# Kernel tuning notes

Hardware: AMD Instinct MI355X
Metric: run time of the kernel (lower is better)

Reference implementation:

```python
import jax, jax.numpy as jnp
import numpy as np

B, LQ, LK, NF = 8, 8192, 1024, 64


def setup_inputs() -> dict:
    key = jax.random.key(0)
    k1, k2, k3, k4, k5 = jax.random.split(key, 5)
    x = jax.random.normal(k1, (B, LQ, NF), dtype=jnp.float32)
    kv = jax.random.normal(k2, (B, LK, NF), dtype=jnp.float32)
    # 1x1 submanifold convolutions == per-point linear maps (no bias)
    scale = 1.0 / np.sqrt(NF)
    Wq = jax.random.normal(k3, (NF, NF), dtype=jnp.float32) * scale
    Wk = jax.random.normal(k4, (NF, NF), dtype=jnp.float32) * scale
    Wv = jax.random.normal(k5, (NF, NF), dtype=jnp.float32) * scale
    return {"x": x, "kv": kv, "Wq": Wq, "Wk": Wk, "Wv": Wv}


def reference(x, kv, Wq, Wk, Wv):
    # q/k/v projections (1x1 convs on sparse features = dense matmuls)
    q = jnp.einsum("bqd,de->bqe", x, Wq)    # [B, LQ, NF]
    k = jnp.einsum("bkd,de->bke", kv, Wk)   # [B, LK, NF]
    v = jnp.einsum("bkd,de->bke", kv, Wv)   # [B, LK, NF]
    # per-batch (block-diagonal / ragged) attention: e = q k^T, softmax over keys, @ v
    scores = jnp.einsum("bqe,bke->bqk", q, k)        # [B, LQ, LK] (no scaling, as in source)
    attn = jax.nn.softmax(scores, axis=-1)
    out = jnp.einsum("bqk,bke->bqe", attn, v)        # [B, LQ, NF]
    return out
```

## Files before the change

kernel.cpp:

```cpp
#include <hip/hip_runtime.h>
#include <hip/hip_fp16.h>

constexpr int B_  = 8;
constexpr int LQ  = 8192;
constexpr int LK  = 1024;
constexpr int NF  = 64;
constexpr int PAD = 8;
constexpr int LDW = NF + PAD;

typedef _Float16 f16x8 __attribute__((ext_vector_type(8)));
typedef float    f32x4 __attribute__((ext_vector_type(4)));

#define MFMA16(a, b, c) __builtin_amdgcn_mfma_f32_16x16x32_f16((a), (b), (c), 0, 0, 0)

__device__ __forceinline__ f16x8 cvt8(const float* p) {
  float4 a = ((const float4*)p)[0];
  float4 b = ((const float4*)p)[1];
  f16x8 r;
  r[0] = (_Float16)a.x; r[1] = (_Float16)a.y; r[2] = (_Float16)a.z; r[3] = (_Float16)a.w;
  r[4] = (_Float16)b.x; r[5] = (_Float16)b.y; r[6] = (_Float16)b.z; r[7] = (_Float16)b.w;
  return r;
}

__device__ __forceinline__ f16x8 ldf(const _Float16* p) { return *(const f16x8*)p; }

__device__ __forceinline__ void st_pk4(_Float16* dst, float a, float b, float c, float d) {
  auto lo = __builtin_amdgcn_cvt_pkrtz(a, b);
  auto hi = __builtin_amdgcn_cvt_pkrtz(c, d);
  auto v  = __builtin_shufflevector(lo, hi, 0, 1, 2, 3);
  *(decltype(v)*)dst = v;
}

__device__ __forceinline__ f16x8 pack8(f32x4 u, f32x4 v) {
  auto a  = __builtin_amdgcn_cvt_pkrtz(u[0], u[1]);
  auto b  = __builtin_amdgcn_cvt_pkrtz(u[2], u[3]);
  auto cc = __builtin_amdgcn_cvt_pkrtz(v[0], v[1]);
  auto d  = __builtin_amdgcn_cvt_pkrtz(v[2], v[3]);
  f16x8 r;
  r[0] = a[0];  r[1] = a[1];  r[2] = b[0]; r[3] = b[1];
  r[4] = cc[0]; r[5] = cc[1]; r[6] = d[0]; r[7] = d[1];
  return r;
}

__device__ __forceinline__ void dma16(const _Float16* g, _Float16* l) {
  __builtin_amdgcn_global_load_lds(
      (const __attribute__((address_space(1))) unsigned int*)g,
      (__attribute__((address_space(3))) unsigned int*)l, 16, 0, 0);
}

__global__ __launch_bounds__(256) void kv_proj_kernel(
    const float* __restrict__ kv, const float* __restrict__ Wk,
    const float* __restrict__ Wv, _Float16* __restrict__ Kb,
    _Float16* __restrict__ Vt) {
  __shared__ __align__(16) _Float16 wkT[NF][LDW];
  __shared__ __align__(16) _Float16 wvT[NF][LDW];
  __shared__ __align__(16) _Float16 ktile[64][LDW];
  __shared__ __align__(16) _Float16 vtileT[64][LDW];

  const int t    = threadIdx.x;
  const int wave = t >> 6, lane = t & 63, g = lane >> 4, c = lane & 15;
  const int b    = blockIdx.x >> 4;
  const int key_base = (blockIdx.x & 15) * 64;

#pragma unroll
  for (int i = 0; i < 16; ++i) {
    int idx = t + 256 * i;
    int e = idx >> 6, d = idx & 63;
    wkT[d][e] = (_Float16)Wk[idx];
    wvT[d][e] = (_Float16)Wv[idx];
  }

  const float* src = kv + ((size_t)b * LK + key_base + wave * 16 + c) * NF;
  f16x8 a0 = cvt8(src + g * 8);
  f16x8 a1 = cvt8(src + 32 + g * 8);
  __syncthreads();

#pragma unroll
  for (int mb = 0; mb < 4; ++mb) {
    f32x4 kacc = {0.f, 0.f, 0.f, 0.f};
    const _Float16* wk0 = &wkT[mb * 16 + c][g * 8];
    kacc = MFMA16(ldf(wk0),      a0, kacc);
    kacc = MFMA16(ldf(wk0 + 32), a1, kacc);
    st_pk4(&ktile[wave * 16 + c][(8 * (mb >> 1) + 2 * g + (mb & 1)) * 4],
           kacc[0], kacc[1], kacc[2], kacc[3]);

    f32x4 vacc = {0.f, 0.f, 0.f, 0.f};
    const _Float16* wv0 = &wvT[mb * 16 + c][g * 8];
    vacc = MFMA16(a0, ldf(wv0),      vacc);
    vacc = MFMA16(a1, ldf(wv0 + 32), vacc);
    st_pk4(&vtileT[mb * 16 + c][(8 * (wave >> 1) + 2 * g + (wave & 1)) * 4],
           vacc[0], vacc[1], vacc[2], vacc[3]);
  }
  __syncthreads();

  _Float16* KbT = Kb + (size_t)blockIdx.x * 4096;
  _Float16* VbT = Vt + (size_t)blockIdx.x * 4096;
#pragma unroll
  for (int rep = 0; rep < 2; ++rep) {
    int q  = t + rep * 256;
    int li = q & 63;
    int gg = li >> 4, cc = li & 15;
    int kb = (q >> 6) & 3, h = q >> 8;
    *(f16x8*)(KbT + q * 8) = ldf(&ktile[kb * 16 + cc][32 * h + 8 * gg]);
    *(f16x8*)(VbT + q * 8) = ldf(&vtileT[kb * 16 + cc][32 * h + 8 * gg]);
  }
}

__global__ __launch_bounds__(256) void attn_kernel(
    const float* __restrict__ x, const float* __restrict__ Wq,
    const _Float16* __restrict__ Kb, const _Float16* __restrict__ Vt,
    float* __restrict__ out) {
  __shared__ __align__(16) _Float16 wq[NF][LDW];
  __shared__ __align__(16) _Float16 tiles[2][8192];

  const int t    = threadIdx.x;
  const int wave = t >> 6, lane = t & 63, g = lane >> 4, c = lane & 15;
  const int b    = blockIdx.x >> 6;
  const int q_base = (blockIdx.x & 63) * 128;
  constexpr float LOG2E = 1.44269504088896f;

  const _Float16* Kt = Kb + (size_t)b * 16 * 4096;
  const _Float16* Vg = Vt + (size_t)b * 16 * 4096;

#pragma unroll
  for (int i = 0; i < 16; ++i) {
    int idx = t + 256 * i;
    wq[idx & 63][idx >> 6] = (_Float16)(Wq[idx] * LOG2E);
  }

#pragma unroll
  for (int q = 0; q < 4; ++q) {
    int ch = wave * 4 + q;
    const _Float16* src = (ch < 8 ? Kt + ch * 512 : Vg + ch * 512 - 4096) + lane * 8;
    dma16(src, &tiles[0][ch * 512]);
  }
  __syncthreads();

  f16x8 qb[2][2];
#pragma unroll
  for (int s = 0; s < 2; ++s) {
    const float* xrow = x + ((size_t)b * LQ + q_base + wave * 32 + s * 16 + c) * NF;
    f16x8 xa0 = cvt8(xrow + g * 8);
    f16x8 xa1 = cvt8(xrow + 32 + g * 8);
    f32x4 qa[4];
#pragma unroll
    for (int mb = 0; mb < 4; ++mb) {
      qa[mb] = {0.f, 0.f, 0.f, 0.f};
      const _Float16* wq0 = &wq[mb * 16 + c][g * 8];
      qa[mb] = MFMA16(ldf(wq0),      xa0, qa[mb]);
      qa[mb] = MFMA16(ldf(wq0 + 32), xa1, qa[mb]);
    }
    qb[s][0] = pack8(qa[0], qa[1]);
    qb[s][1] = pack8(qa[2], qa[3]);
  }

  float m_s[2] = {-1e30f, -1e30f}, l_s[2] = {0.f, 0.f};
  f32x4 oacc[2][4];
#pragma unroll
  for (int s = 0; s < 2; ++s)
#pragma unroll
    for (int nb = 0; nb < 4; ++nb) oacc[s][nb] = {0.f, 0.f, 0.f, 0.f};

#pragma unroll 2
  for (int tile = 0; tile < 16; ++tile) {
    const int buf = tile & 1;
    if (tile < 15) {
      const _Float16* kn = Kt + (tile + 1) * 4096;
      const _Float16* vn = Vg + (tile + 1) * 4096;
#pragma unroll
      for (int q = 0; q < 4; ++q) {
        int ch = wave * 4 + q;
        const _Float16* src = (ch < 8 ? kn + ch * 512 : vn + ch * 512 - 4096) + lane * 8;
        dma16(src, &tiles[buf ^ 1][ch * 512]);
      }
    }
    const _Float16* tb = tiles[buf];

    f32x4 st[2][4];
#pragma unroll
    for (int kb = 0; kb < 4; ++kb) {
      f16x8 k0 = ldf(tb + (size_t)(kb * 64 + lane) * 8);
      f16x8 k1 = ldf(tb + (size_t)((kb + 4) * 64 + lane) * 8);
      st[0][kb] = {0.f, 0.f, 0.f, 0.f};
      st[1][kb] = {0.f, 0.f, 0.f, 0.f};
      st[0][kb] = MFMA16(k0, qb[0][0], st[0][kb]);
      st[0][kb] = MFMA16(k1, qb[0][1], st[0][kb]);
      st[1][kb] = MFMA16(k0, qb[1][0], st[1][kb]);
      st[1][kb] = MFMA16(k1, qb[1][1], st[1][kb]);
    }

    f16x8 pa[2][2];
#pragma unroll
    for (int s = 0; s < 2; ++s) {
      float tmax = st[s][0][0];
#pragma unroll
      for (int kb = 0; kb < 4; ++kb)
#pragma unroll
        for (int r = 0; r < 4; ++r) tmax = fmaxf(tmax, st[s][kb][r]);
      tmax = fmaxf(tmax, __shfl_xor(tmax, 16));
      tmax = fmaxf(tmax, __shfl_xor(tmax, 32));

      if (__ballot(tmax > m_s[s]) != 0) {
        float mnew  = fmaxf(m_s[s], tmax);
        float alpha = __builtin_amdgcn_exp2f(m_s[s] - mnew);
        m_s[s] = mnew;
        l_s[s] *= alpha;
        float aq[4];
#pragma unroll
        for (int r = 0; r < 4; ++r) aq[r] = __shfl(alpha, 4 * g + r);
#pragma unroll
        for (int nb = 0; nb < 4; ++nb)
#pragma unroll
          for (int r = 0; r < 4; ++r) oacc[s][nb][r] *= aq[r];
      }

      float rsum = 0.f;
#pragma unroll
      for (int kb = 0; kb < 4; ++kb)
#pragma unroll
        for (int r = 0; r < 4; ++r) {
          float p = __builtin_amdgcn_exp2f(st[s][kb][r] - m_s[s]);
          st[s][kb][r] = p;
          rsum += p;
        }
      rsum += __shfl_xor(rsum, 16);
      rsum += __shfl_xor(rsum, 32);
      l_s[s] += rsum;

      pa[s][0] = pack8(st[s][0], st[s][1]);
      pa[s][1] = pack8(st[s][2], st[s][3]);
    }

#pragma unroll
    for (int nb = 0; nb < 4; ++nb) {
      f16x8 v0 = ldf(tb + 4096 + (size_t)(nb * 64 + lane) * 8);
      f16x8 v1 = ldf(tb + 4096 + (size_t)((nb + 4) * 64 + lane) * 8);
      oacc[0][nb] = MFMA16(pa[0][0], v0, oacc[0][nb]);
      oacc[0][nb] = MFMA16(pa[0][1], v1, oacc[0][nb]);
      oacc[1][nb] = MFMA16(pa[1][0], v0, oacc[1][nb]);
      oacc[1][nb] = MFMA16(pa[1][1], v1, oacc[1][nb]);
    }
    __syncthreads();
  }

#pragma unroll
  for (int s = 0; s < 2; ++s) {
    float linv = 1.0f / l_s[s];
    float lq[4];
#pragma unroll
    for (int r = 0; r < 4; ++r) lq[r] = __shfl(linv, 4 * g + r);
#pragma unroll
    for (int nb = 0; nb < 4; ++nb)
#pragma unroll
      for (int r = 0; r < 4; ++r)
        out[((size_t)b * LQ + q_base + wave * 32 + s * 16 + 4 * g + r) * NF + nb * 16 + c] =
            oacc[s][nb][r] * lq[r];
  }
}

extern "C" void kernel_launch(void* const* d_in, const int* in_sizes, int n_in,
                              void* d_out, int out_size, void* d_ws, size_t ws_size,
                              hipStream_t stream) {
  const float* x  = (const float*)d_in[0];
  const float* kv = (const float*)d_in[1];
  const float* Wq = (const float*)d_in[2];
  const float* Wk = (const float*)d_in[3];
  const float* Wv = (const float*)d_in[4];
  float* out = (float*)d_out;

  _Float16* Kb = (_Float16*)d_ws;
  _Float16* Vt = Kb + (size_t)B_ * LK * NF;

  kv_proj_kernel<<<B_ * (LK / 64), 256, 0, stream>>>(kv, Wk, Wv, Kb, Vt);
  attn_kernel<<<B_ * (LQ / 128), 256, 0, stream>>>(x, Wq, Kb, Vt, out);
}
```

Measured before the change: 108.7 us.

## Use 128-key tiles with interleaved KV layout and MFMA row-sum

The projection kernel now writes K and V into one interleaved buffer laid out as 128-key tiles, so the attention kernel streams one contiguous 32KB chunk per tile and runs 8 iterations instead of 16. The softmax row sum is computed with an MFMA against a ones vector instead of scalar adds and cross-lane shuffles. The trailing __syncthreads is replaced by a waitcnt+barrier at loop start, and Wq staging reuses the second LDS buffer. The aim is fewer barriers and fewer rescale passes per key, plus less VALU and shuffle work, at the cost of more registers for larger score tiles and 64KB of LDS, which may lower occupancy.

```diff
diff --git a/kernel.cpp b/kernel.cpp
--- a/kernel.cpp
+++ b/kernel.cpp
@@ -48,10 +48,13 @@
       (__attribute__((address_space(3))) unsigned int*)l, 16, 0, 0);
 }
 
+__device__ __forceinline__ void tile_barrier() {
+  asm volatile("s_waitcnt vmcnt(0)\n\ts_barrier" ::: "memory");
+}
+
 __global__ __launch_bounds__(256) void kv_proj_kernel(
     const float* __restrict__ kv, const float* __restrict__ Wk,
-    const float* __restrict__ Wv, _Float16* __restrict__ Kb,
-    _Float16* __restrict__ Vt) {
+    const float* __restrict__ Wv, _Float16* __restrict__ KV) {
   __shared__ __align__(16) _Float16 wkT[NF][LDW];
   __shared__ __align__(16) _Float16 wvT[NF][LDW];
   __shared__ __align__(16) _Float16 ktile[64][LDW];
@@ -60,7 +63,8 @@
   const int t    = threadIdx.x;
   const int wave = t >> 6, lane = t & 63, g = lane >> 4, c = lane & 15;
   const int b    = blockIdx.x >> 4;
-  const int key_base = (blockIdx.x & 15) * 64;
+  const int t64  = blockIdx.x & 15;
+  const int key_base = t64 * 64;
 
 #pragma unroll
   for (int i = 0; i < 16; ++i) {
@@ -93,25 +97,25 @@
   }
   __syncthreads();
 
-  _Float16* KbT = Kb + (size_t)blockIdx.x * 4096;
-  _Float16* VbT = Vt + (size_t)blockIdx.x * 4096;
+  const int half = t64 & 1;
+  _Float16* base = KV + ((size_t)b * 8 + (t64 >> 1)) * 16384;
 #pragma unroll
   for (int rep = 0; rep < 2; ++rep) {
-    int q  = t + rep * 256;
-    int li = q & 63;
-    int gg = li >> 4, cc = li & 15;
-    int kb = (q >> 6) & 3, h = q >> 8;
-    *(f16x8*)(KbT + q * 8) = ldf(&ktile[kb * 16 + cc][32 * h + 8 * gg]);
-    *(f16x8*)(VbT + q * 8) = ldf(&vtileT[kb * 16 + cc][32 * h + 8 * gg]);
+    int q   = t + rep * 256;
+    int li  = q & 63;
+    int gg  = li >> 4, cc = li & 15;
+    int sub = (q >> 6) & 3, h = q >> 8;
+    int ck  = h * 8 + half * 4 + sub;
+    int cv  = (half * 2 + h) * 4 + sub;
+    *(f16x8*)(base + (ck * 64 + li) * 8)        = ldf(&ktile[sub * 16 + cc][32 * h + 8 * gg]);
+    *(f16x8*)(base + 8192 + (cv * 64 + li) * 8) = ldf(&vtileT[sub * 16 + cc][32 * h + 8 * gg]);
   }
 }
 
 __global__ __launch_bounds__(256) void attn_kernel(
     const float* __restrict__ x, const float* __restrict__ Wq,
-    const _Float16* __restrict__ Kb, const _Float16* __restrict__ Vt,
-    float* __restrict__ out) {
-  __shared__ __align__(16) _Float16 wq[NF][LDW];
-  __shared__ __align__(16) _Float16 tiles[2][8192];
+    const _Float16* __restrict__ KV, float* __restrict__ out) {
+  __shared__ __align__(16) _Float16 lds[2][16384];
 
   const int t    = threadIdx.x;
   const int wave = t >> 6, lane = t & 63, g = lane >> 4, c = lane & 15;
@@ -119,20 +123,18 @@
   const int q_base = (blockIdx.x & 63) * 128;
   constexpr float LOG2E = 1.44269504088896f;
 
-  const _Float16* Kt = Kb + (size_t)b * 16 * 4096;
-  const _Float16* Vg = Vt + (size_t)b * 16 * 4096;
-
+  _Float16* wqp = &lds[1][0];
 #pragma unroll
   for (int i = 0; i < 16; ++i) {
     int idx = t + 256 * i;
-    wq[idx & 63][idx >> 6] = (_Float16)(Wq[idx] * LOG2E);
-  }
-
-#pragma unroll
-  for (int q = 0; q < 4; ++q) {
-    int ch = wave * 4 + q;
-    const _Float16* src = (ch < 8 ? Kt + ch * 512 : Vg + ch * 512 - 4096) + lane * 8;
-    dma16(src, &tiles[0][ch * 512]);
+    wqp[(idx & 63) * LDW + (idx >> 6)] = (_Float16)(Wq[idx] * LOG2E);
+  }
+
+  const _Float16* Kt = KV + (size_t)b * 8 * 16384;
+#pragma unroll
+  for (int q = 0; q < 8; ++q) {
+    int ch = wave * 8 + q;
+    dma16(Kt + ch * 512 + lane * 8, &lds[0][ch * 512]);
   }
   __syncthreads();
 
@@ -146,7 +148,7 @@
 #pragma unroll
     for (int mb = 0; mb < 4; ++mb) {
       qa[mb] = {0.f, 0.f, 0.f, 0.f};
-      const _Float16* wq0 = &wq[mb * 16 + c][g * 8];
+      const _Float16* wq0 = &wqp[(mb * 16 + c) * LDW + g * 8];
       qa[mb] = MFMA16(ldf(wq0),      xa0, qa[mb]);
       qa[mb] = MFMA16(ldf(wq0 + 32), xa1, qa[mb]);
     }
@@ -154,33 +156,36 @@
     qb[s][1] = pack8(qa[2], qa[3]);
   }
 
-  float m_s[2] = {-1e30f, -1e30f}, l_s[2] = {0.f, 0.f};
+  f16x8 ones;
+#pragma unroll
+  for (int j = 0; j < 8; ++j) ones[j] = (_Float16)1.0f;
+
+  float m_s[2] = {-1e30f, -1e30f};
+  f32x4 lacc[2] = {{0.f, 0.f, 0.f, 0.f}, {0.f, 0.f, 0.f, 0.f}};
   f32x4 oacc[2][4];
 #pragma unroll
   for (int s = 0; s < 2; ++s)
 #pragma unroll
     for (int nb = 0; nb < 4; ++nb) oacc[s][nb] = {0.f, 0.f, 0.f, 0.f};
 
-#pragma unroll 2
-  for (int tile = 0; tile < 16; ++tile) {
-    const int buf = tile & 1;
-    if (tile < 15) {
-      const _Float16* kn = Kt + (tile + 1) * 4096;
-      const _Float16* vn = Vg + (tile + 1) * 4096;
-#pragma unroll
-      for (int q = 0; q < 4; ++q) {
-        int ch = wave * 4 + q;
-        const _Float16* src = (ch < 8 ? kn + ch * 512 : vn + ch * 512 - 4096) + lane * 8;
-        dma16(src, &tiles[buf ^ 1][ch * 512]);
+  for (int tile = 0; tile < 8; ++tile) {
+    tile_barrier();
+    if (tile < 7) {
+      const _Float16* nt = Kt + (size_t)(tile + 1) * 16384;
+      _Float16* nb_ = &lds[(tile + 1) & 1][0];
+#pragma unroll
+      for (int q = 0; q < 8; ++q) {
+        int ch = wave * 8 + q;
+        dma16(nt + ch * 512 + lane * 8, nb_ + ch * 512);
       }
     }
-    const _Float16* tb = tiles[buf];
-
-    f32x4 st[2][4];
-#pragma unroll
-    for (int kb = 0; kb < 4; ++kb) {
+    const _Float16* tb = &lds[tile & 1][0];
+
+    f32x4 st[2][8];
+#pragma unroll
+    for (int kb = 0; kb < 8; ++kb) {
       f16x8 k0 = ldf(tb + (size_t)(kb * 64 + lane) * 8);
-      f16x8 k1 = ldf(tb + (size_t)((kb + 4) * 64 + lane) * 8);
+      f16x8 k1 = ldf(tb + (size_t)((8 + kb) * 64 + lane) * 8);
       st[0][kb] = {0.f, 0.f, 0.f, 0.f};
       st[1][kb] = {0.f, 0.f, 0.f, 0.f};
       st[0][kb] = MFMA16(k0, qb[0][0], st[0][kb]);
@@ -189,12 +194,12 @@
       st[1][kb] = MFMA16(k1, qb[1][1], st[1][kb]);
     }
 
-    f16x8 pa[2][2];
+    f16x8 pa[2][4];
 #pragma unroll
     for (int s = 0; s < 2; ++s) {
       float tmax = st[s][0][0];
 #pragma unroll
-      for (int kb = 0; kb < 4; ++kb)
+      for (int kb = 0; kb < 8; ++kb)
 #pragma unroll
         for (int r = 0; r < 4; ++r) tmax = fmaxf(tmax, st[s][kb][r]);
       tmax = fmaxf(tmax, __shfl_xor(tmax, 16));
@@ -204,57 +209,54 @@
         float mnew  = fmaxf(m_s[s], tmax);
         float alpha = __builtin_amdgcn_exp2f(m_s[s] - mnew);
         m_s[s] = mnew;
-        l_s[s] *= alpha;
         float aq[4];
 #pragma unroll
         for (int r = 0; r < 4; ++r) aq[r] = __shfl(alpha, 4 * g + r);
+#pragma unroll
+        for (int r = 0; r < 4; ++r) lacc[s][r] *= aq[r];
 #pragma unroll
         for (int nb = 0; nb < 4; ++nb)
 #pragma unroll
           for (int r = 0; r < 4; ++r) oacc[s][nb][r] *= aq[r];
       }
 
-      float rsum = 0.f;
-#pragma unroll
-      for (int kb = 0; kb < 4; ++kb)
-#pragma unroll
-        for (int r = 0; r < 4; ++r) {
-          float p = __builtin_amdgcn_exp2f(st[s][kb][r] - m_s[s]);
-          st[s][kb][r] = p;
-          rsum += p;
-        }
-      rsum += __shfl_xor(rsum, 16);
-      rsum += __shfl_xor(rsum, 32);
-      l_s[s] += rsum;
-
-      pa[s][0] = pack8(st[s][0], st[s][1]);
-      pa[s][1] = pack8(st[s][2], st[s][3]);
+#pragma unroll
+      for (int kb = 0; kb < 8; ++kb)
+#pragma unroll
+        for (int r = 0; r < 4; ++r)
+          st[s][kb][r] = __builtin_amdgcn_exp2f(st[s][kb][r] - m_s[s]);
+
+#pragma unroll
+      for (int hh = 0; hh < 4; ++hh)
+        pa[s][hh] = pack8(st[s][2 * hh], st[s][2 * hh + 1]);
+
+#pragma unroll
+      for (int hh = 0; hh < 4; ++hh)
+        lacc[s] = MFMA16(pa[s][hh], ones, lacc[s]);
     }
 
 #pragma unroll
     for (int nb = 0; nb < 4; ++nb) {
-      f16x8 v0 = ldf(tb + 4096 + (size_t)(nb * 64 + lane) * 8);
-      f16x8 v1 = ldf(tb + 4096 + (size_t)((nb + 4) * 64 + lane) * 8);
-      oacc[0][nb] = MFMA16(pa[0][0], v0, oacc[0][nb]);
-      oacc[0][nb] = MFMA16(pa[0][1], v1, oacc[0][nb]);
-      oacc[1][nb] = MFMA16(pa[1][0], v0, oacc[1][nb]);
-      oacc[1][nb] = MFMA16(pa[1][1], v1, oacc[1][nb]);
-    }
-    __syncthreads();
+#pragma unroll
+      for (int hh = 0; hh < 4; ++hh) {
+        f16x8 vf = ldf(tb + 8192 + (size_t)((hh * 4 + nb) * 64 + lane) * 8);
+        oacc[0][nb] = MFMA16(pa[0][hh], vf, oacc[0][nb]);
+        oacc[1][nb] = MFMA16(pa[1][hh], vf, oacc[1][nb]);
+      }
+    }
   }
 
 #pragma unroll
   for (int s = 0; s < 2; ++s) {
-    float linv = 1.0f / l_s[s];
-    float lq[4];
-#pragma unroll
-    for (int r = 0; r < 4; ++r) lq[r] = __shfl(linv, 4 * g + r);
+    float linv[4];
+#pragma unroll
+    for (int r = 0; r < 4; ++r) linv[r] = 1.0f / lacc[s][r];
 #pragma unroll
     for (int nb = 0; nb < 4; ++nb)
 #pragma unroll
       for (int r = 0; r < 4; ++r)
         out[((size_t)b * LQ + q_base + wave * 32 + s * 16 + 4 * g + r) * NF + nb * 16 + c] =
-            oacc[s][nb][r] * lq[r];
+            oacc[s][nb][r] * linv[r];
   }
 }
 
@@ -268,9 +270,8 @@
   const float* Wv = (const float*)d_in[4];
   float* out = (float*)d_out;
 
-  _Float16* Kb = (_Float16*)d_ws;
-  _Float16* Vt = Kb + (size_t)B_ * LK * NF;
-
-  kv_proj_kernel<<<B_ * (LK / 64), 256, 0, stream>>>(kv, Wk, Wv, Kb, Vt);
-  attn_kernel<<<B_ * (LQ / 128), 256, 0, stream>>>(x, Wq, Kb, Vt, out);
-}
+  _Float16* KV = (_Float16*)d_ws;
+
+  kv_proj_kernel<<<B_ * (LK / 64), 256, 0, stream>>>(kv, Wk, Wv, KV);
+  attn_kernel<<<B_ * (LQ / 128), 256, 0, stream>>>(x, Wq, KV, out);
+}
```

Result: faster. 104.2 us (-4.2%).
